# Performance work log

Measured on AMD Instinct MI355X. Metric: run time of the kernel, lower is better.

## Reference

```python
import jax, jax.numpy as jnp
import numpy as np

N_A, N_B = 50000, 10000
E = 300000
IN_F, HID, BEL_OUT, INC_OUT = 256, 256, 128, 128


def _gconv(x_src, W, b, src, dst, n_src, n_dst):
    """DGL GraphConv with norm='both': D_in^{-1/2} A D_out^{-1/2} X W + b, degs clamped to >=1."""
    ones = jnp.ones(src.shape[0], x_src.dtype)
    deg_out = jnp.maximum(jax.ops.segment_sum(ones, src, num_segments=n_src), 1.0)
    deg_in = jnp.maximum(jax.ops.segment_sum(ones, dst, num_segments=n_dst), 1.0)
    h = (x_src * jax.lax.rsqrt(deg_out)[:, None]) @ W        # [n_src, out]
    agg = jax.ops.segment_sum(h[src], dst, num_segments=n_dst)  # scatter-add messages
    return agg * jax.lax.rsqrt(deg_in)[:, None] + b


def setup_inputs() -> dict:
    key = jax.random.key(0)
    ks = jax.random.split(key, 12)
    s = 1.0 / np.sqrt(IN_F)
    sh = 1.0 / np.sqrt(HID)
    return {
        "x_a": jax.random.normal(ks[0], (N_A, IN_F), jnp.float32),
        "x_b": jax.random.normal(ks[1], (N_B, IN_F), jnp.float32),
        "W1_bel": jax.random.normal(ks[2], (IN_F, HID), jnp.float32) * s,
        "b1_bel": jnp.zeros((HID,), jnp.float32),
        "W1_inc": jax.random.normal(ks[3], (IN_F, HID), jnp.float32) * s,
        "b1_inc": jnp.zeros((HID,), jnp.float32),
        "W2_bel": jax.random.normal(ks[4], (HID, BEL_OUT), jnp.float32) * sh,
        "b2_bel": jnp.zeros((BEL_OUT,), jnp.float32),
        "W2_inc": jax.random.normal(ks[5], (HID, INC_OUT), jnp.float32) * sh,
        "b2_inc": jnp.zeros((INC_OUT,), jnp.float32),
        "bel_src": jax.random.randint(ks[6], (E,), 0, N_A, jnp.int32),
        "bel_dst": jax.random.randint(ks[7], (E,), 0, N_B, jnp.int32),
        "inc_src": jax.random.randint(ks[8], (E,), 0, N_B, jnp.int32),
        "inc_dst": jax.random.randint(ks[9], (E,), 0, N_A, jnp.int32),
    }


def reference(x_a, x_b, W1_bel, b1_bel, W1_inc, b1_inc, W2_bel, b2_bel,
              W2_inc, b2_inc, bel_src, bel_dst, inc_src, inc_dst):
    n_a, n_b = x_a.shape[0], x_b.shape[0]
    # layer 1 (HeteroGraphConv, mean over a single relation per dst type = identity)
    h_b = _gconv(x_a, W1_bel, b1_bel, bel_src, bel_dst, n_a, n_b)  # 'belongs_to': A->B
    h_a = _gconv(x_b, W1_inc, b1_inc, inc_src, inc_dst, n_b, n_a)  # 'including' : B->A
    h_a = jax.nn.relu(h_a)
    h_b = jax.nn.relu(h_b)
    # layer 2
    out_b = _gconv(h_a, W2_bel, b2_bel, bel_src, bel_dst, n_a, n_b)  # [N_B, bel_out]
    out_a = _gconv(h_b, W2_inc, b2_inc, inc_src, inc_dst, n_b, n_a)  # [N_A, inc_out]
    return out_a, out_b
```

## Files before the change

kernel.cpp:

```cpp
#include <hip/hip_runtime.h>


#define NA 50000
#define NB 10000
#define NE 300000
#define GB 625
#define HB 1172
#define PB 64
#define CB 300

typedef unsigned short u16;
typedef unsigned int u32;
typedef __attribute__((ext_vector_type(8))) short short8;
typedef __attribute__((ext_vector_type(4))) float f32x4;
typedef __attribute__((ext_vector_type(2))) float f32x2;
typedef __attribute__((ext_vector_type(4))) unsigned short u16x4;
typedef __attribute__((ext_vector_type(4))) int i32x4;

__device__ __forceinline__ float bf2f(u16 h){
  union { u32 u; float f; } x; x.u = ((u32)h) << 16; return x.f;
}
__device__ __forceinline__ u16 f2bf(float f){
  union { float f; u32 u; } x; x.f = f;
  u32 r = (x.u + 0x7FFFu + ((x.u >> 16) & 1u)) >> 16;
  return (u16)r;
}

__device__ __forceinline__ void pack_elem(int t,
    const float* __restrict__ W1b, const float* __restrict__ W1i,
    const float* __restrict__ W2b, const float* __restrict__ W2i,
    u16* __restrict__ pwh, u16* __restrict__ pwl){
  const float* W; int N; int tt;
  if (t < 65536)       { W = W1b; N = 256; tt = t; }
  else if (t < 131072) { W = W1i; N = 256; tt = t - 65536; }
  else if (t < 163840) { W = W2b; N = 128; tt = t - 131072; }
  else                 { W = W2i; N = 128; tt = t - 163840; }
  int j = tt & 7, lane = (tt >> 3) & 63, tile = tt >> 9;
  int nT = N >> 4;
  int nt = tile % nT, kt = tile / nT;
  int k = kt * 32 + ((lane >> 4) << 3) + j;
  int n = nt * 16 + (lane & 15);
  float v = W[k * N + n];
  u16 hi = f2bf(v);
  pwh[t] = hi;
  pwl[t] = f2bf(v - bf2f(hi));
}

__global__ __launch_bounds__(256) void pre_kernel(
    int* __restrict__ z, int nz4, const float* __restrict__ W1i,
    u16* __restrict__ pwh, u16* __restrict__ pwl){
  int g = blockIdx.x * blockDim.x + threadIdx.x;
  int s = gridDim.x * blockDim.x;
  i32x4* z4 = (i32x4*)z;
  i32x4 zero = {0, 0, 0, 0};
  for (int i = g; i < nz4; i += s) __builtin_nontemporal_store(zero, z4 + i);
  for (int t = g; t < 65536; t += s)
    pack_elem(65536 + t, nullptr, W1i, nullptr, nullptr, pwh, pwl);
}

__device__ __forceinline__ void gemm_dev(int blk, const float* __restrict__ A,
                                         const u16* __restrict__ PWH,
                                         const u16* __restrict__ PWL,
                                         const float* __restrict__ bias,
                                         const float* __restrict__ rs,
                                         float* __restrict__ Cf,
                                         u16* __restrict__ C16,
                                         int M, int nT, int wpsShift,
                                         int doRelu, int ldC, int colOff){
  int wave = blk * 4 + (threadIdx.x >> 6);
  int lane = threadIdx.x & 63;
  int strips = M >> 4;
  int strip = wave >> wpsShift;
  if (strip >= strips) return;
  int slice = wave & ((1 << wpsShift) - 1);
  int ntPer = nT >> wpsShift;
  int ntStart = slice * ntPer;
  int r16 = lane & 15, quad = lane >> 4;
  int m0 = strip << 4;
  const float* aBase = A + (size_t)(m0 + r16) * 256 + quad * 8;
  short8 ah[8], al[8];
#pragma unroll
  for (int kt = 0; kt < 8; ++kt){
    float4 p0 = *(const float4*)(aBase + kt * 32);
    float4 p1 = *(const float4*)(aBase + kt * 32 + 4);
    float v[8] = {p0.x, p0.y, p0.z, p0.w, p1.x, p1.y, p1.z, p1.w};
    short8 h, l;
#pragma unroll
    for (int j = 0; j < 8; ++j){
      u16 hb = f2bf(v[j]);
      h[j] = (short)hb;
      l[j] = (short)f2bf(v[j] - bf2f(hb));
    }
    ah[kt] = h; al[kt] = l;
  }
  float rscale[4];
#pragma unroll
  for (int r = 0; r < 4; ++r) rscale[r] = rs ? rs[m0 + quad * 4 + r] : 1.f;
  for (int nt = ntStart; nt < ntStart + ntPer; ++nt){
    f32x4 acc = {0.f, 0.f, 0.f, 0.f};
    const u16* bh = PWH + ((size_t)nt * 64 + lane) * 8;
    const u16* bl = PWL + ((size_t)nt * 64 + lane) * 8;
#pragma unroll
    for (int kt = 0; kt < 8; ++kt){
      short8 wh = *(const short8*)(bh + (size_t)kt * nT * 512);
      short8 wl = *(const short8*)(bl + (size_t)kt * nT * 512);
      acc = __builtin_amdgcn_mfma_f32_16x16x32_bf16(ah[kt], wh, acc, 0, 0, 0);
      acc = __builtin_amdgcn_mfma_f32_16x16x32_bf16(al[kt], wh, acc, 0, 0, 0);
      acc = __builtin_amdgcn_mfma_f32_16x16x32_bf16(ah[kt], wl, acc, 0, 0, 0);
    }
    int col = nt * 16 + r16;
    float bv = bias ? bias[col] : 0.f;
#pragma unroll
    for (int r = 0; r < 4; ++r){
      float v = acc[r] * rscale[r] + bv;
      if (doRelu) v = fmaxf(v, 0.f);
      size_t o = (size_t)(m0 + quad * 4 + r) * ldC + colOff + col;
      if (C16) __builtin_nontemporal_store(f2bf(v), C16 + o);
      else     __builtin_nontemporal_store(v, Cf + o);
    }
  }
}

__global__ __launch_bounds__(256) void mega_kernel(
    const float* __restrict__ xb,
    const u16* __restrict__ WH1i, const u16* __restrict__ WL1i,
    u16* __restrict__ G12,
    const int* __restrict__ bs, const int* __restrict__ bd,
    const int* __restrict__ isc, const int* __restrict__ idt,
    int* __restrict__ c_bs, int* __restrict__ c_bd4,
    int* __restrict__ c_is4, int* __restrict__ c_id,
    int* __restrict__ rank_bel, int* __restrict__ rank_inc,
    const float* __restrict__ W1b, const float* __restrict__ W2b,
    const float* __restrict__ W2i,
    u16* __restrict__ pwh, u16* __restrict__ pwl,
    const float* __restrict__ xa, u16* __restrict__ xa16){
  int blk = blockIdx.x;
  if (blk < GB){
    gemm_dev(blk, xb, WH1i, WL1i, nullptr, nullptr,
             nullptr, G12, NB, 16, 2, 0, 384, 0);
  } else if (blk < GB + HB){
    int g = (blk - GB) * blockDim.x + threadIdx.x;
    int s = HB * blockDim.x;
    for (int e = g; e < NE; e += s){
      int r = e & 3;
      atomicAdd(&c_bs[bs[e]], 1);
      rank_bel[e] = atomicAdd(&c_bd4[bd[e] * 4 + r], 1);
      atomicAdd(&c_is4[isc[e] * 4 + r], 1);
      rank_inc[e] = atomicAdd(&c_id[idt[e]], 1);
    }
  } else if (blk < GB + HB + PB){
    int g = (blk - GB - HB) * blockDim.x + threadIdx.x;
    int s = PB * blockDim.x;
    for (int v = g; v < 131072; v += s){
      int t = v < 65536 ? v : v + 65536;
      pack_elem(t, W1b, nullptr, W2b, W2i, pwh, pwl);
    }
  } else {
    int g = ((blk - GB - HB - PB) * blockDim.x + threadIdx.x) * 4;
    int s = CB * blockDim.x * 4;
    for (int i = g; i < NA * 256; i += s){
      float4 v = *(const float4*)(xa + i);
      u16x4 o;
      o.x = f2bf(v.x); o.y = f2bf(v.y); o.z = f2bf(v.z); o.w = f2bf(v.w);
      __builtin_nontemporal_store(o, (u16x4*)(xa16 + i));
    }
  }
}

template<int SEG>
__device__ __forceinline__ void scan_block(const int* __restrict__ cnt,
                                           int* __restrict__ off, int n){
  __shared__ int wsum[16];
  int tid = threadIdx.x, lane = tid & 63, wid = tid >> 6;
  int i0 = tid * SEG;
  int v[SEG];
#pragma unroll
  for (int r = 0; r < SEG; ++r){
    int idx = i0 + r;
    v[r] = (idx < n) ? cnt[idx] : 0;
  }
  int sum = 0;
#pragma unroll
  for (int r = 0; r < SEG; ++r) sum += v[r];
  int x = sum;
#pragma unroll
  for (int d = 1; d < 64; d <<= 1){
    int t = __shfl_up(x, d, 64);
    if (lane >= d) x += t;
  }
  if (lane == 63) wsum[wid] = x;
  __syncthreads();
  if (wid == 0){
    int ws = (lane < 16) ? wsum[lane] : 0;
#pragma unroll
    for (int d = 1; d < 16; d <<= 1){
      int t = __shfl_up(ws, d, 64);
      if (lane >= d) ws += t;
    }
    if (lane < 16) wsum[lane] = ws;
  }
  __syncthreads();
  int run = (wid ? wsum[wid - 1] : 0) + (x - sum);
#pragma unroll
  for (int r = 0; r < SEG; ++r){
    int idx = i0 + r;
    if (idx < n) off[idx] = run;
    run += v[r];
  }
  if (tid == 0) off[n] = wsum[15];
}

__global__ __launch_bounds__(1024) void scan_scales_kernel(
    const int* __restrict__ c_bs, const int* __restrict__ c_bd4,
    const int* __restrict__ c_is4, const int* __restrict__ c_id,
    int* __restrict__ off_bel4, int* __restrict__ off_inc,
    float* __restrict__ s_ob, float* __restrict__ s_ib,
    float* __restrict__ s_oi, float* __restrict__ s_ii){
  if (blockIdx.x >= 2){
    int g = (blockIdx.x - 2) * blockDim.x + threadIdx.x;
    int s = (gridDim.x - 2) * blockDim.x;
    for (int i = g; i < NA; i += s){
      int a = c_bs[i]; s_ob[i] = rsqrtf((float)(a > 1 ? a : 1));
      int b = c_id[i]; s_ii[i] = rsqrtf((float)(b > 1 ? b : 1));
      if (i < NB){
        i32x4 cb = *(const i32x4*)(c_bd4 + i * 4);
        int c = cb[0] + cb[1] + cb[2] + cb[3];
        s_ib[i] = rsqrtf((float)(c > 1 ? c : 1));
        i32x4 ci = *(const i32x4*)(c_is4 + i * 4);
        int d = ci[0] + ci[1] + ci[2] + ci[3];
        s_oi[i] = rsqrtf((float)(d > 1 ? d : 1));
      }
    }
    return;
  }
  if (blockIdx.x == 0) scan_block<40>(c_bd4, off_bel4, 40000);
  else                 scan_block<49>(c_id, off_inc, NA);
}

__global__ __launch_bounds__(256) void fill_kernel(
    const int* __restrict__ bs, const int* __restrict__ bd,
    const int* __restrict__ isc, const int* __restrict__ idt,
    const int* __restrict__ rank_bel, const int* __restrict__ rank_inc,
    const int* __restrict__ off_bel4, const int* __restrict__ off_inc,
    int* __restrict__ csr_bel, int* __restrict__ csr_inc){
  int g = blockIdx.x * blockDim.x + threadIdx.x;
  int s = gridDim.x * blockDim.x;
  for (int e = g; e < NE; e += s){
    int r = e & 3;
    csr_bel[off_bel4[bd[e] * 4 + r] + rank_bel[e]] = bs[e];
    csr_inc[off_inc[idt[e]] + rank_inc[e]] = isc[e];
  }
}

__global__ __launch_bounds__(256) void agg_bel_kernel(
    const u16* __restrict__ X, const float* __restrict__ ss,
    const int* __restrict__ off4, const int* __restrict__ csr,
    float* __restrict__ Pf, int nDst){
  int wave = blockIdx.x * 4 + (threadIdx.x >> 6);
  int lane = threadIdx.x & 63;
  if (wave >= nDst) return;
  int b0 = off4[wave * 4], b1 = off4[wave * 4 + 4];
  int deg = b1 - b0;
  int part = lane >> 5;
  int cl = lane & 31;
  int c = cl * 8;
  float acc[8];
#pragma unroll
  for (int q = 0; q < 8; ++q) acc[q] = 0.f;
  int idx = 0; float sc = 0.f;
  if (lane < deg){
    idx = csr[b0 + lane];
    sc = ss ? ss[idx] : 1.f;
  }
  int lim = deg < 64 ? deg : 64;
  for (int u = 0; u < lim; u += 8){
    const u16* addr[4]; float w[4];
#pragma unroll
    for (int k = 0; k < 4; ++k){
      int e = u + k * 2 + part;
      int t = e < lim ? e : 0;
      int s0 = __shfl(idx, t, 64);
      float c0 = __shfl(sc, t, 64);
      w[k] = e < lim ? c0 : 0.f;
      addr[k] = X + (size_t)s0 * 256 + c;
    }
    short8 v[4];
#pragma unroll
    for (int k = 0; k < 4; ++k) v[k] = *(const short8*)addr[k];
#pragma unroll
    for (int k = 0; k < 4; ++k)
#pragma unroll
      for (int q = 0; q < 8; ++q) acc[q] += bf2f((u16)v[k][q]) * w[k];
  }
  for (int j = b0 + 64 + part; j < b1; j += 2){
    int s0 = csr[j];
    float c0 = ss ? ss[s0] : 1.f;
    short8 v0 = *(const short8*)(X + (size_t)s0 * 256 + c);
#pragma unroll
    for (int q = 0; q < 8; ++q) acc[q] += bf2f((u16)v0[q]) * c0;
  }
#pragma unroll
  for (int q = 0; q < 8; ++q) acc[q] += __shfl_xor(acc[q], 32, 64);
  if (part == 0){
    f32x4 f0 = {acc[0], acc[1], acc[2], acc[3]};
    f32x4 f1 = {acc[4], acc[5], acc[6], acc[7]};
    __builtin_nontemporal_store(f0, (f32x4*)(Pf + (size_t)wave * 256 + c));
    __builtin_nontemporal_store(f1, (f32x4*)(Pf + (size_t)wave * 256 + c + 4));
  }
}

__global__ __launch_bounds__(256) void gemmHG_kernel(
    const float* __restrict__ Pb,
    const u16* __restrict__ WH1b, const u16* __restrict__ WL1b,
    const float* __restrict__ b1b, const float* __restrict__ s_ib,
    const u16* __restrict__ WH2i, const u16* __restrict__ WL2i,
    u16* __restrict__ G12){
  __shared__ float Hs[16][260];
  int w = threadIdx.x >> 6;
  int lane = threadIdx.x & 63;
  int r16 = lane & 15, quad = lane >> 4;
  int m0 = blockIdx.x << 4;
  const float* aBase = Pb + (size_t)(m0 + r16) * 256 + quad * 8;
  short8 ah[8], al[8];
#pragma unroll
  for (int kt = 0; kt < 8; ++kt){
    float4 p0 = *(const float4*)(aBase + kt * 32);
    float4 p1 = *(const float4*)(aBase + kt * 32 + 4);
    float v[8] = {p0.x, p0.y, p0.z, p0.w, p1.x, p1.y, p1.z, p1.w};
    short8 h, l;
#pragma unroll
    for (int j = 0; j < 8; ++j){
      u16 hb = f2bf(v[j]);
      h[j] = (short)hb;
      l[j] = (short)f2bf(v[j] - bf2f(hb));
    }
    ah[kt] = h; al[kt] = l;
  }
  float rs1[4];
#pragma unroll
  for (int r = 0; r < 4; ++r) rs1[r] = s_ib[m0 + quad * 4 + r];
  for (int nt = w * 4; nt < w * 4 + 4; ++nt){
    f32x4 acc = {0.f, 0.f, 0.f, 0.f};
    const u16* bh = WH1b + ((size_t)nt * 64 + lane) * 8;
    const u16* bl = WL1b + ((size_t)nt * 64 + lane) * 8;
#pragma unroll
    for (int kt = 0; kt < 8; ++kt){
      short8 wh = *(const short8*)(bh + (size_t)kt * 16 * 512);
      short8 wl = *(const short8*)(bl + (size_t)kt * 16 * 512);
      acc = __builtin_amdgcn_mfma_f32_16x16x32_bf16(ah[kt], wh, acc, 0, 0, 0);
      acc = __builtin_amdgcn_mfma_f32_16x16x32_bf16(al[kt], wh, acc, 0, 0, 0);
      acc = __builtin_amdgcn_mfma_f32_16x16x32_bf16(ah[kt], wl, acc, 0, 0, 0);
    }
    int col = nt * 16 + r16;
    float bv = b1b[col];
#pragma unroll
    for (int r = 0; r < 4; ++r)
      Hs[quad * 4 + r][col] = fmaxf(acc[r] * rs1[r] + bv, 0.f);
  }
  __syncthreads();
  short8 ah2[8], al2[8];
#pragma unroll
  for (int kt = 0; kt < 8; ++kt){
    float4 p0 = *(const float4*)&Hs[r16][kt * 32 + quad * 8];
    float4 p1 = *(const float4*)&Hs[r16][kt * 32 + quad * 8 + 4];
    float v[8] = {p0.x, p0.y, p0.z, p0.w, p1.x, p1.y, p1.z, p1.w};
    short8 h, l;
#pragma unroll
    for (int j = 0; j < 8; ++j){
      u16 hb = f2bf(v[j]);
      h[j] = (short)hb;
      l[j] = (short)f2bf(v[j] - bf2f(hb));
    }
    ah2[kt] = h; al2[kt] = l;
  }
  for (int nt = w * 2; nt < w * 2 + 2; ++nt){
    f32x4 acc = {0.f, 0.f, 0.f, 0.f};
    const u16* bh = WH2i + ((size_t)nt * 64 + lane) * 8;
    const u16* bl = WL2i + ((size_t)nt * 64 + lane) * 8;
#pragma unroll
    for (int kt = 0; kt < 8; ++kt){
      short8 wh = *(const short8*)(bh + (size_t)kt * 8 * 512);
      short8 wl = *(const short8*)(bl + (size_t)kt * 8 * 512);
      acc = __builtin_amdgcn_mfma_f32_16x16x32_bf16(ah2[kt], wh, acc, 0, 0, 0);
      acc = __builtin_amdgcn_mfma_f32_16x16x32_bf16(al2[kt], wh, acc, 0, 0, 0);
      acc = __builtin_amdgcn_mfma_f32_16x16x32_bf16(ah2[kt], wl, acc, 0, 0, 0);
    }
    int col = nt * 16 + r16;
#pragma unroll
    for (int r = 0; r < 4; ++r){
      u16 o = f2bf(acc[r]);
      __builtin_nontemporal_store(o, G12 + (size_t)(m0 + quad * 4 + r) * 384 + 256 + col);
    }
  }
}

__global__ __launch_bounds__(256) void agg_inc2_kernel(
    const u16* __restrict__ G12, const int* __restrict__ off,
    const int* __restrict__ csr, const float* __restrict__ s_oi,
    const float* __restrict__ s_ii, const float* __restrict__ s_ob,
    const float* __restrict__ b1i, const float* __restrict__ b2i,
    u16* __restrict__ Ha, float* __restrict__ outa){
  int wave = blockIdx.x * 4 + (threadIdx.x >> 6);
  int lane = threadIdx.x & 63;
  if (wave >= NA) return;
  int b0 = off[wave], b1 = off[wave + 1];
  int deg = b1 - b0;
  int c1 = lane * 4;
  int c2 = lane * 2;
  float acc[6];
#pragma unroll
  for (int q = 0; q < 6; ++q) acc[q] = 0.f;
  int idx = 0; float sc = 0.f;
  if (lane < deg){
    idx = csr[b0 + lane];
    sc = s_oi[idx];
  }
  int lim = deg < 64 ? deg : 64;
  for (int u = 0; u < lim; u += 4){
    ushort4 va[4]; ushort2 vb[4]; float w[4];
#pragma unroll
    for (int k = 0; k < 4; ++k){
      int e = u + k;
      int t = e < lim ? e : 0;
      int se = __shfl(idx, t, 64);
      float c0 = __shfl(sc, t, 64);
      w[k] = e < lim ? c0 : 0.f;
      const u16* r = G12 + (size_t)se * 384;
      va[k] = *(const ushort4*)(r + c1);
      vb[k] = *(const ushort2*)(r + 256 + c2);
    }
#pragma unroll
    for (int k = 0; k < 4; ++k){
      acc[0] += bf2f(va[k].x) * w[k];
      acc[1] += bf2f(va[k].y) * w[k];
      acc[2] += bf2f(va[k].z) * w[k];
      acc[3] += bf2f(va[k].w) * w[k];
      acc[4] += bf2f(vb[k].x) * w[k];
      acc[5] += bf2f(vb[k].y) * w[k];
    }
  }
  for (int j = b0 + 64; j < b1; ++j){
    int se = csr[j];
    float c0 = s_oi[se];
    const u16* r = G12 + (size_t)se * 384;
    ushort4 va = *(const ushort4*)(r + c1);
    ushort2 vb = *(const ushort2*)(r + 256 + c2);
    acc[0] += bf2f(va.x) * c0; acc[1] += bf2f(va.y) * c0;
    acc[2] += bf2f(va.z) * c0; acc[3] += bf2f(va.w) * c0;
    acc[4] += bf2f(vb.x) * c0; acc[5] += bf2f(vb.y) * c0;
  }
  float sii = s_ii[wave], sob = s_ob[wave];
  float4 bb1 = *(const float4*)(b1i + c1);
  f32x2 bb2 = *(const f32x2*)(b2i + c2);
  u16x4 o1;
  o1.x = f2bf(fmaxf(acc[0] * sii + bb1.x, 0.f) * sob);
  o1.y = f2bf(fmaxf(acc[1] * sii + bb1.y, 0.f) * sob);
  o1.z = f2bf(fmaxf(acc[2] * sii + bb1.z, 0.f) * sob);
  o1.w = f2bf(fmaxf(acc[3] * sii + bb1.w, 0.f) * sob);
  __builtin_nontemporal_store(o1, (u16x4*)(Ha + (size_t)wave * 256 + c1));
  f32x2 o2 = {acc[4] * sii + bb2.x, acc[5] * sii + bb2.y};
  __builtin_nontemporal_store(o2, (f32x2*)(outa + (size_t)wave * 128 + c2));
}

__global__ __launch_bounds__(256) void gemm_kernel(
    const float* __restrict__ A,
    const u16* __restrict__ PWH, const u16* __restrict__ PWL,
    const float* __restrict__ bias, const float* __restrict__ rs,
    float* __restrict__ Cf, u16* __restrict__ C16,
    int M, int nT, int wpsShift, int doRelu, int ldC, int colOff){
  gemm_dev(blockIdx.x, A, PWH, PWL, bias, rs, Cf, C16,
           M, nT, wpsShift, doRelu, ldC, colOff);
}

extern "C" void kernel_launch(void* const* d_in, const int* in_sizes, int n_in,
                              void* d_out, int out_size, void* d_ws, size_t ws_size,
                              hipStream_t stream){
  const float* x_a = (const float*)d_in[0];
  const float* x_b = (const float*)d_in[1];
  const float* W1b = (const float*)d_in[2];
  const float* b1b = (const float*)d_in[3];
  const float* W1i = (const float*)d_in[4];
  const float* b1i = (const float*)d_in[5];
  const float* W2b = (const float*)d_in[6];
  const float* b2b = (const float*)d_in[7];
  const float* W2i = (const float*)d_in[8];
  const float* b2i = (const float*)d_in[9];
  const int* bs  = (const int*)d_in[10];
  const int* bd  = (const int*)d_in[11];
  const int* isc = (const int*)d_in[12];
  const int* idt = (const int*)d_in[13];

  char* w = (char*)d_ws;
  size_t o = 0;
  auto take = [&](size_t bytes) -> void* {
    void* p = w + o; o = (o + bytes + 255) & ~(size_t)255; return p;
  };
  int* zint = (int*)take((size_t)180000 * sizeof(int));
  int* c_bs  = zint;
  int* c_bd4 = zint + 50000;
  int* c_is4 = zint + 90000;
  int* c_id  = zint + 130000;
  int* rank_bel = (int*)take(NE * sizeof(int));
  int* rank_inc = (int*)take(NE * sizeof(int));
  int* off_bel4 = (int*)take((40000 + 1) * sizeof(int));
  int* off_inc  = (int*)take((NA + 1) * sizeof(int));
  int* csr_bel = (int*)take(NE * sizeof(int));
  int* csr_inc = (int*)take(NE * sizeof(int));
  float* s_ob = (float*)take(NA * sizeof(float));
  float* s_ib = (float*)take(NB * sizeof(float));
  float* s_oi = (float*)take(NB * sizeof(float));
  float* s_ii = (float*)take(NA * sizeof(float));
  u16* pwh = (u16*)take(196608 * sizeof(u16));
  u16* pwl = (u16*)take(196608 * sizeof(u16));
  u16* pwh1b = pwh, *pwh1i = pwh + 65536, *pwh2b = pwh + 131072, *pwh2i = pwh + 163840;
  u16* pwl1b = pwl, *pwl1i = pwl + 65536, *pwl2b = pwl + 131072, *pwl2i = pwl + 163840;
  u16* xa16 = (u16*)take((size_t)NA * 256 * sizeof(u16));
  u16* G12  = (u16*)take((size_t)NB * 384 * sizeof(u16));
  u16* H_a  = (u16*)take((size_t)NA * 256 * sizeof(u16));
  float* P_b = (float*)take((size_t)NB * 256 * sizeof(float));

  float* out_a = (float*)d_out;
  float* out_b = (float*)d_out + (size_t)NA * 128;

  pre_kernel<<<256, 256, 0, stream>>>(zint, 180000 / 4, W1i, pwh, pwl);
  mega_kernel<<<GB + HB + PB + CB, 256, 0, stream>>>(
      x_b, pwh1i, pwl1i, G12,
      bs, bd, isc, idt, c_bs, c_bd4, c_is4, c_id, rank_bel, rank_inc,
      W1b, W2b, W2i, pwh, pwl, x_a, xa16);
  scan_scales_kernel<<<52, 1024, 0, stream>>>(c_bs, c_bd4, c_is4, c_id,
                                              off_bel4, off_inc,
                                              s_ob, s_ib, s_oi, s_ii);
  fill_kernel<<<1172, 256, 0, stream>>>(bs, bd, isc, idt, rank_bel, rank_inc,
                                        off_bel4, off_inc, csr_bel, csr_inc);
  agg_bel_kernel<<<2500, 256, 0, stream>>>(xa16, s_ob, off_bel4, csr_bel, P_b, NB);
  gemmHG_kernel<<<625, 256, 0, stream>>>(P_b, pwh1b, pwl1b, b1b, s_ib,
                                         pwh2i, pwl2i, G12);
  agg_inc2_kernel<<<12500, 256, 0, stream>>>(G12, off_inc, csr_inc, s_oi,
                                             s_ii, s_ob, b1i, b2i, H_a, out_a);
  agg_bel_kernel<<<2500, 256, 0, stream>>>(H_a, nullptr, off_bel4, csr_bel, P_b, NB);
  gemm_kernel<<<625, 256, 0, stream>>>(P_b, pwh2b, pwl2b, b2b, s_ib,
                                       out_b, nullptr, NB, 8, 2, 0, 128, 0);
}
```

Baseline: 363.5 us.

## Use per-XCC degree counter slots with workgroup-scope atomics

The degree-counting phase now gives each XCC its own counter slot (8 slots per node) for three of the four counters. It uses relaxed workgroup-scope atomics, so each XCC's increments can stay in its local L2 instead of contending device-wide. The XCC id is packed into the top bits of rank_bel. The scan, fill and aggregation kernels are updated to use the 8-slot offsets. In exchange the zeroed counter buffer grows from 180000 to 610000 ints, the scan input grows, and correctness depends on cross-XCC writeback of partially written cache lines at kernel boundaries.

```diff
diff --git a/kernel.cpp b/kernel.cpp
--- a/kernel.cpp
+++ b/kernel.cpp
@@ -16,6 +16,10 @@
 typedef __attribute__((ext_vector_type(2))) float f32x2;
 typedef __attribute__((ext_vector_type(4))) unsigned short u16x4;
 typedef __attribute__((ext_vector_type(4))) int i32x4;
+
+__device__ __forceinline__ int xcc_id(){
+  return (int)(__builtin_amdgcn_s_getreg(63508) & 7u);
+}
 
 __device__ __forceinline__ float bf2f(u16 h){
   union { u32 u; float f; } x; x.u = ((u32)h) << 16; return x.f;
@@ -127,8 +131,8 @@
     u16* __restrict__ G12,
     const int* __restrict__ bs, const int* __restrict__ bd,
     const int* __restrict__ isc, const int* __restrict__ idt,
-    int* __restrict__ c_bs, int* __restrict__ c_bd4,
-    int* __restrict__ c_is4, int* __restrict__ c_id,
+    int* __restrict__ c_bs8, int* __restrict__ c_bd8,
+    int* __restrict__ c_is8, int* __restrict__ c_id,
     int* __restrict__ rank_bel, int* __restrict__ rank_inc,
     const float* __restrict__ W1b, const float* __restrict__ W2b,
     const float* __restrict__ W2i,
@@ -139,13 +143,17 @@
     gemm_dev(blk, xb, WH1i, WL1i, nullptr, nullptr,
              nullptr, G12, NB, 16, 2, 0, 384, 0);
   } else if (blk < GB + HB){
+    int xcc = xcc_id();
     int g = (blk - GB) * blockDim.x + threadIdx.x;
     int s = HB * blockDim.x;
     for (int e = g; e < NE; e += s){
-      int r = e & 3;
-      atomicAdd(&c_bs[bs[e]], 1);
-      rank_bel[e] = atomicAdd(&c_bd4[bd[e] * 4 + r], 1);
-      atomicAdd(&c_is4[isc[e] * 4 + r], 1);
+      __hip_atomic_fetch_add(&c_bs8[bs[e] * 8 + xcc], 1,
+                             __ATOMIC_RELAXED, __HIP_MEMORY_SCOPE_WORKGROUP);
+      int rb = __hip_atomic_fetch_add(&c_bd8[bd[e] * 8 + xcc], 1,
+                             __ATOMIC_RELAXED, __HIP_MEMORY_SCOPE_WORKGROUP);
+      rank_bel[e] = rb | (xcc << 27);
+      __hip_atomic_fetch_add(&c_is8[isc[e] * 8 + xcc], 1,
+                             __ATOMIC_RELAXED, __HIP_MEMORY_SCOPE_WORKGROUP);
       rank_inc[e] = atomicAdd(&c_id[idt[e]], 1);
     }
   } else if (blk < GB + HB + PB){
@@ -211,29 +219,34 @@
 }
 
 __global__ __launch_bounds__(1024) void scan_scales_kernel(
-    const int* __restrict__ c_bs, const int* __restrict__ c_bd4,
-    const int* __restrict__ c_is4, const int* __restrict__ c_id,
-    int* __restrict__ off_bel4, int* __restrict__ off_inc,
+    const int* __restrict__ c_bs8, const int* __restrict__ c_bd8,
+    const int* __restrict__ c_is8, const int* __restrict__ c_id,
+    int* __restrict__ off_bel8, int* __restrict__ off_inc,
     float* __restrict__ s_ob, float* __restrict__ s_ib,
     float* __restrict__ s_oi, float* __restrict__ s_ii){
   if (blockIdx.x >= 2){
     int g = (blockIdx.x - 2) * blockDim.x + threadIdx.x;
     int s = (gridDim.x - 2) * blockDim.x;
     for (int i = g; i < NA; i += s){
-      int a = c_bs[i]; s_ob[i] = rsqrtf((float)(a > 1 ? a : 1));
+      i32x4 a0 = *(const i32x4*)(c_bs8 + i * 8);
+      i32x4 a1 = *(const i32x4*)(c_bs8 + i * 8 + 4);
+      int a = a0[0] + a0[1] + a0[2] + a0[3] + a1[0] + a1[1] + a1[2] + a1[3];
+      s_ob[i] = rsqrtf((float)(a > 1 ? a : 1));
       int b = c_id[i]; s_ii[i] = rsqrtf((float)(b > 1 ? b : 1));
       if (i < NB){
-        i32x4 cb = *(const i32x4*)(c_bd4 + i * 4);
-        int c = cb[0] + cb[1] + cb[2] + cb[3];
+        i32x4 c0 = *(const i32x4*)(c_bd8 + i * 8);
+        i32x4 c1 = *(const i32x4*)(c_bd8 + i * 8 + 4);
+        int c = c0[0] + c0[1] + c0[2] + c0[3] + c1[0] + c1[1] + c1[2] + c1[3];
         s_ib[i] = rsqrtf((float)(c > 1 ? c : 1));
-        i32x4 ci = *(const i32x4*)(c_is4 + i * 4);
-        int d = ci[0] + ci[1] + ci[2] + ci[3];
+        i32x4 d0 = *(const i32x4*)(c_is8 + i * 8);
+        i32x4 d1 = *(const i32x4*)(c_is8 + i * 8 + 4);
+        int d = d0[0] + d0[1] + d0[2] + d0[3] + d1[0] + d1[1] + d1[2] + d1[3];
         s_oi[i] = rsqrtf((float)(d > 1 ? d : 1));
       }
     }
     return;
   }
-  if (blockIdx.x == 0) scan_block<40>(c_bd4, off_bel4, 40000);
+  if (blockIdx.x == 0) scan_block<79>(c_bd8, off_bel8, NB * 8);
   else                 scan_block<49>(c_id, off_inc, NA);
 }
 
@@ -241,25 +254,27 @@
     const int* __restrict__ bs, const int* __restrict__ bd,
     const int* __restrict__ isc, const int* __restrict__ idt,
     const int* __restrict__ rank_bel, const int* __restrict__ rank_inc,
-    const int* __restrict__ off_bel4, const int* __restrict__ off_inc,
+    const int* __restrict__ off_bel8, const int* __restrict__ off_inc,
     int* __restrict__ csr_bel, int* __restrict__ csr_inc){
   int g = blockIdx.x * blockDim.x + threadIdx.x;
   int s = gridDim.x * blockDim.x;
   for (int e = g; e < NE; e += s){
-    int r = e & 3;
-    csr_bel[off_bel4[bd[e] * 4 + r] + rank_bel[e]] = bs[e];
+    int pb = rank_bel[e];
+    int xcc = pb >> 27;
+    int rb = pb & ((1 << 27) - 1);
+    csr_bel[off_bel8[bd[e] * 8 + xcc] + rb] = bs[e];
     csr_inc[off_inc[idt[e]] + rank_inc[e]] = isc[e];
   }
 }
 
 __global__ __launch_bounds__(256) void agg_bel_kernel(
     const u16* __restrict__ X, const float* __restrict__ ss,
-    const int* __restrict__ off4, const int* __restrict__ csr,
+    const int* __restrict__ off8, const int* __restrict__ csr,
     float* __restrict__ Pf, int nDst){
   int wave = blockIdx.x * 4 + (threadIdx.x >> 6);
   int lane = threadIdx.x & 63;
   if (wave >= nDst) return;
-  int b0 = off4[wave * 4], b1 = off4[wave * 4 + 4];
+  int b0 = off8[wave * 8], b1 = off8[wave * 8 + 8];
   int deg = b1 - b0;
   int part = lane >> 5;
   int cl = lane & 31;
@@ -495,14 +510,14 @@
   auto take = [&](size_t bytes) -> void* {
     void* p = w + o; o = (o + bytes + 255) & ~(size_t)255; return p;
   };
-  int* zint = (int*)take((size_t)180000 * sizeof(int));
-  int* c_bs  = zint;
-  int* c_bd4 = zint + 50000;
-  int* c_is4 = zint + 90000;
-  int* c_id  = zint + 130000;
+  int* zint = (int*)take((size_t)610000 * sizeof(int));
+  int* c_bs8 = zint;
+  int* c_bd8 = zint + 400000;
+  int* c_is8 = zint + 480000;
+  int* c_id  = zint + 560000;
   int* rank_bel = (int*)take(NE * sizeof(int));
   int* rank_inc = (int*)take(NE * sizeof(int));
-  int* off_bel4 = (int*)take((40000 + 1) * sizeof(int));
+  int* off_bel8 = (int*)take((NB * 8 + 1) * sizeof(int));
   int* off_inc  = (int*)take((NA + 1) * sizeof(int));
   int* csr_bel = (int*)take(NE * sizeof(int));
   int* csr_inc = (int*)take(NE * sizeof(int));
@@ -522,22 +537,22 @@
   float* out_a = (float*)d_out;
   float* out_b = (float*)d_out + (size_t)NA * 128;
 
-  pre_kernel<<<256, 256, 0, stream>>>(zint, 180000 / 4, W1i, pwh, pwl);
+  pre_kernel<<<256, 256, 0, stream>>>(zint, 610000 / 4, W1i, pwh, pwl);
   mega_kernel<<<GB + HB + PB + CB, 256, 0, stream>>>(
       x_b, pwh1i, pwl1i, G12,
-      bs, bd, isc, idt, c_bs, c_bd4, c_is4, c_id, rank_bel, rank_inc,
+      bs, bd, isc, idt, c_bs8, c_bd8, c_is8, c_id, rank_bel, rank_inc,
       W1b, W2b, W2i, pwh, pwl, x_a, xa16);
-  scan_scales_kernel<<<52, 1024, 0, stream>>>(c_bs, c_bd4, c_is4, c_id,
-                                              off_bel4, off_inc,
+  scan_scales_kernel<<<52, 1024, 0, stream>>>(c_bs8, c_bd8, c_is8, c_id,
+                                              off_bel8, off_inc,
                                               s_ob, s_ib, s_oi, s_ii);
   fill_kernel<<<1172, 256, 0, stream>>>(bs, bd, isc, idt, rank_bel, rank_inc,
-                                        off_bel4, off_inc, csr_bel, csr_inc);
-  agg_bel_kernel<<<2500, 256, 0, stream>>>(xa16, s_ob, off_bel4, csr_bel, P_b, NB);
+                                        off_bel8, off_inc, csr_bel, csr_inc);
+  agg_bel_kernel<<<2500, 256, 0, stream>>>(xa16, s_ob, off_bel8, csr_bel, P_b, NB);
   gemmHG_kernel<<<625, 256, 0, stream>>>(P_b, pwh1b, pwl1b, b1b, s_ib,
                                          pwh2i, pwl2i, G12);
   agg_inc2_kernel<<<12500, 256, 0, stream>>>(G12, off_inc, csr_inc, s_oi,
                                              s_ii, s_ob, b1i, b2i, H_a, out_a);
-  agg_bel_kernel<<<2500, 256, 0, stream>>>(H_a, nullptr, off_bel4, csr_bel, P_b, NB);
+  agg_bel_kernel<<<2500, 256, 0, stream>>>(H_a, nullptr, off_bel8, csr_bel, P_b, NB);
   gemm_kernel<<<625, 256, 0, stream>>>(P_b, pwh2b, pwl2b, b2b, s_ib,
                                        out_b, nullptr, NB, 8, 2, 0, 128, 0);
 }
```

New measurement: 410.5 us. 1.13x slower.
